# Performance work log

Measured on AMD Instinct MI355X. Metric: run time of the kernel, lower is better.

Reference implementation:

```python
import jax, jax.numpy as jnp
import numpy as np

N = 65536          # nodes
E = 1048576        # edges
IN_C = 128
HID_C = 32
HEADS = 4
OUT_C = 64
NEG_SLOPE = 0.2
EPS = 1e-16


def gat_conv(x, edge_index, W, att_src, att_dst, bias, heads, out_c, concat):
    """PyG-style GATConv. x: [N, F_in]; edge_index: [2, E] (row=src, col=dst).
    W: [F_in, heads*out_c]; att_src/att_dst: [heads, out_c]; bias: [heads*out_c] or [out_c]."""
    src, dst = edge_index[0], edge_index[1]
    n = x.shape[0]
    h = (x @ W).reshape(n, heads, out_c)                      # [N, H, C]
    a_src = jnp.einsum('nhc,hc->nh', h, att_src)              # [N, H]
    a_dst = jnp.einsum('nhc,hc->nh', h, att_dst)              # [N, H]
    alpha = a_src[src] + a_dst[dst]                           # [E, H]
    alpha = jax.nn.leaky_relu(alpha, NEG_SLOPE)
    # segment softmax over incoming edges of each destination node
    amax = jax.ops.segment_max(alpha, dst, num_segments=n)    # [N, H]
    alpha = jnp.exp(alpha - amax[dst])
    denom = jax.ops.segment_sum(alpha, dst, num_segments=n)   # [N, H]
    alpha = alpha / (denom[dst] + EPS)
    # weighted scatter-add aggregation
    msgs = alpha[:, :, None] * h[src]                         # [E, H, C]
    out = jax.ops.segment_sum(msgs, dst, num_segments=n)      # [N, H, C]
    if concat:
        out = out.reshape(n, heads * out_c)
    else:
        out = out.mean(axis=1)
    return out + bias


def setup_inputs() -> dict:
    key = jax.random.key(0)
    ks = jax.random.split(key, 10)
    s_in = 1.0 / np.sqrt(IN_C)
    s_h = 1.0 / np.sqrt(HEADS * HID_C)
    x = jax.random.normal(ks[0], (N, IN_C), dtype=jnp.float32)
    edge_index = jax.random.randint(ks[1], (2, E), 0, N, dtype=jnp.int64)
    W1 = jax.random.normal(ks[2], (IN_C, HEADS * HID_C), dtype=jnp.float32) * s_in
    att_src1 = jax.random.normal(ks[3], (HEADS, HID_C), dtype=jnp.float32) * s_h
    att_dst1 = jax.random.normal(ks[4], (HEADS, HID_C), dtype=jnp.float32) * s_h
    b1 = jnp.zeros((HEADS * HID_C,), dtype=jnp.float32)
    W2 = jax.random.normal(ks[5], (HEADS * HID_C, OUT_C), dtype=jnp.float32) * s_h
    att_src2 = jax.random.normal(ks[6], (1, OUT_C), dtype=jnp.float32) * s_h
    att_dst2 = jax.random.normal(ks[7], (1, OUT_C), dtype=jnp.float32) * s_h
    b2 = jnp.zeros((OUT_C,), dtype=jnp.float32)
    return {"x": x, "edge_index": edge_index, "W1": W1, "att_src1": att_src1,
            "att_dst1": att_dst1, "b1": b1, "W2": W2, "att_src2": att_src2,
            "att_dst2": att_dst2, "b2": b2}


def reference(x, edge_index, W1, att_src1, att_dst1, b1, W2, att_src2, att_dst2, b2):
    # dropout is identity in eval mode
    h = gat_conv(x, edge_index, W1, att_src1, att_dst1, b1, HEADS, HID_C, concat=True)
    h = jax.nn.sigmoid(h)
    h = gat_conv(h, edge_index, W2, att_src2, att_dst2, b2, 1, OUT_C, concat=True)
    return jax.nn.sigmoid(h)
```

## Files before the change

kernel.cpp:

```cpp
#include <hip/hip_runtime.h>
#include <hip/hip_fp16.h>

#define N_NODES 65536
#define N_EDGES 1048576
#define NBUCK 256
#define PBLOCKS 1024
#define EPB (N_EDGES / PBLOCKS)
#define K4CAP 6144
constexpr float NEG = 0.2f;
constexpr float EPS_ = 1e-16f;
constexpr float WSHIFT = 2.7725887f;

typedef __attribute__((ext_vector_type(8))) short bf16x8;
typedef __attribute__((ext_vector_type(4))) float f32x4;

__device__ __forceinline__ unsigned short f2bf(float f) {
    unsigned int u = __float_as_uint(f);
    return (unsigned short)((u + 0x7fffu + ((u >> 16) & 1u)) >> 16);
}
__device__ __forceinline__ unsigned short f2h(float f) {
    __half_raw r = __half_raw(__float2half(f));
    return r.x;
}
__device__ __forceinline__ __half2 u2h2(unsigned int u) {
    union { unsigned int u; __half2 h; } c; c.u = u; return c.h;
}
__device__ __forceinline__ unsigned int h22u(__half2 h) {
    union { unsigned int u; __half2 h; } c; c.h = h; return c.u;
}
__device__ __forceinline__ float lrelu_exp_s(float l) {
    return __expf(fmaxf(l, NEG * l) - WSHIFT);
}


__global__ __launch_bounds__(256) void coarse_hist(const int* __restrict__ ei,
                                                   int* __restrict__ hist_mat) {
    __shared__ int h[NBUCK];
    int t = threadIdx.x;
    h[t] = 0;
    __syncthreads();
    int base = blockIdx.x * EPB;
    #pragma unroll
    for (int i = 0; i < EPB / 256; ++i) {
        int d = ei[N_EDGES + base + i * 256 + t];
        atomicAdd(&h[d >> 8], 1);
    }
    __syncthreads();
    hist_mat[t * PBLOCKS + blockIdx.x] = h[t];
}

__global__ __launch_bounds__(1024) void scan_a(const int* __restrict__ in,
                                               int* __restrict__ out,
                                               int* __restrict__ bsum) {
    __shared__ int sm[1024];
    int t = threadIdx.x, i = blockIdx.x * 1024 + t;
    int v = in[i];
    sm[t] = v;
    __syncthreads();
    for (int off = 1; off < 1024; off <<= 1) {
        int u = (t >= off) ? sm[t - off] : 0;
        __syncthreads();
        sm[t] += u;
        __syncthreads();
    }
    out[i] = sm[t] - v;
    if (t == 1023) bsum[blockIdx.x] = sm[t];
}

__global__ __launch_bounds__(256) void scan_b(int* __restrict__ bsum) {
    __shared__ int sm[256];
    int t = threadIdx.x;
    int v = bsum[t];
    sm[t] = v;
    __syncthreads();
    for (int off = 1; off < 256; off <<= 1) {
        int u = (t >= off) ? sm[t - off] : 0;
        __syncthreads();
        sm[t] += u;
        __syncthreads();
    }
    bsum[t] = sm[t] - v;
}

__global__ __launch_bounds__(1024) void scan_c(int* __restrict__ arr,
                                               const int* __restrict__ bsum) {
    int i = blockIdx.x * 1024 + threadIdx.x;
    arr[i] += bsum[blockIdx.x];
}

__global__ __launch_bounds__(256) void partition_kernel(const int* __restrict__ ei,
                                                        const int* __restrict__ cursor_mat,
                                                        unsigned int* __restrict__ edge_part) {
    __shared__ int h[NBUCK];
    __shared__ int start[NBUCK];
    __shared__ int cur[NBUCK];
    __shared__ int gcur[NBUCK];
    __shared__ unsigned int stage[EPB];
    int t = threadIdx.x;
    h[t] = 0;
    gcur[t] = cursor_mat[t * PBLOCKS + blockIdx.x];
    __syncthreads();
    unsigned int ent[EPB / 256];
    int base = blockIdx.x * EPB;
    #pragma unroll
    for (int i = 0; i < EPB / 256; ++i) {
        int e = base + i * 256 + t;
        int s = ei[e], d = ei[N_EDGES + e];
        ent[i] = ((unsigned int)s << 16) | (unsigned int)d;
        atomicAdd(&h[d >> 8], 1);
    }
    __syncthreads();
    int v = h[t];
    start[t] = v;
    __syncthreads();
    for (int off = 1; off < 256; off <<= 1) {
        int u = (t >= off) ? start[t - off] : 0;
        __syncthreads();
        start[t] += u;
        __syncthreads();
    }
    int excl = start[t] - v;
    start[t] = excl;
    cur[t] = excl;
    __syncthreads();
    #pragma unroll
    for (int i = 0; i < EPB / 256; ++i) {
        int b = (int)((ent[i] & 0xffffu) >> 8);
        int slot = atomicAdd(&cur[b], 1);
        stage[slot] = ent[i];
    }
    __syncthreads();
    int s0 = t * (EPB / 256);
    #pragma unroll
    for (int i = 0; i < EPB / 256; ++i) {
        unsigned int p = stage[s0 + i];
        int b = (int)((p & 0xffffu) >> 8);
        edge_part[gcur[b] + (s0 + i - start[b])] = p;
    }
}

__global__ __launch_bounds__(1024) void finalize_kernel(const unsigned int* __restrict__ edge_part,
                                                        const int* __restrict__ cursor_mat,
                                                        int* __restrict__ row_ptr,
                                                        unsigned short* __restrict__ csr16) {
    __shared__ int h[256];
    __shared__ int sc[256];
    __shared__ int cur[256];
    __shared__ unsigned short stage[K4CAP];
    int t = threadIdx.x;
    int b = blockIdx.x;
    if (b == NBUCK - 1 && t == 0) row_ptr[N_NODES] = N_EDGES;
    int cs = cursor_mat[b * PBLOCKS];
    int ce = (b == NBUCK - 1) ? N_EDGES : cursor_mat[(b + 1) * PBLOCKS];
    int cnt = ce - cs;
    if (t < 256) h[t] = 0;
    __syncthreads();
    for (int i = t; i < cnt; i += 1024)
        atomicAdd(&h[edge_part[cs + i] & 0xffu], 1);
    __syncthreads();
    int v = 0;
    if (t < 256) { v = h[t]; sc[t] = v; }
    __syncthreads();
    for (int off = 1; off < 256; off <<= 1) {
        int u = (t < 256 && t >= off) ? sc[t - off] : 0;
        __syncthreads();
        if (t < 256) sc[t] += u;
        __syncthreads();
    }
    if (t < 256) {
        int excl = sc[t] - v;
        row_ptr[b * 256 + t] = cs + excl;
        cur[t] = excl;
    }
    __syncthreads();
    if (cnt <= K4CAP) {
        for (int i = t; i < cnt; i += 1024) {
            unsigned int p = edge_part[cs + i];
            int slot = atomicAdd(&cur[p & 0xffu], 1);
            stage[slot] = (unsigned short)(p >> 16);
        }
        __syncthreads();
        for (int i = t; i < cnt; i += 1024)
            csr16[cs + i] = stage[i];
    } else {
        for (int i = t; i < cnt; i += 1024) {
            unsigned int p = edge_part[cs + i];
            int slot = atomicAdd(&cur[p & 0xffu], 1);
            csr16[cs + slot] = (unsigned short)(p >> 16);
        }
    }
}


__global__ __launch_bounds__(256) void gemm1_mfma(const float* __restrict__ X,
                                                  const float* __restrict__ W,
                                                  unsigned short* __restrict__ H) {
    constexpr int OUTC = 128;
    constexpr int NT = OUTC / 16;
    extern __shared__ unsigned short Wl[];
    int t = threadIdx.x;
    for (int idx = t; idx < OUTC * 128; idx += 256) {
        int j = idx & 7;
        int ln = (idx >> 3) & 63;
        int fc = idx >> 9;
        int kc = fc & 3, ct = fc >> 2;
        int k = kc * 32 + (ln >> 4) * 8 + j;
        int n = ct * 16 + (ln & 15);
        Wl[idx] = (unsigned short)f2bf(W[k * OUTC + n]);
    }
    __syncthreads();
    int wave = t >> 6, lane = t & 63;
    int m = lane & 15, quad = lane >> 4;
    int node_base = blockIdx.x * 64 + wave * 16;
    const float* xrow = X + (size_t)(node_base + m) * 128 + quad * 8;
    bf16x8 a[4];
    #pragma unroll
    for (int kc = 0; kc < 4; ++kc) {
        float4 u = *(const float4*)(xrow + kc * 32);
        float4 v = *(const float4*)(xrow + kc * 32 + 4);
        bf16x8 af;
        af[0] = (short)f2bf(u.x); af[1] = (short)f2bf(u.y);
        af[2] = (short)f2bf(u.z); af[3] = (short)f2bf(u.w);
        af[4] = (short)f2bf(v.x); af[5] = (short)f2bf(v.y);
        af[6] = (short)f2bf(v.z); af[7] = (short)f2bf(v.w);
        a[kc] = af;
    }
    #pragma unroll
    for (int ct = 0; ct < NT; ++ct) {
        f32x4 acc = {0.f, 0.f, 0.f, 0.f};
        #pragma unroll
        for (int kc = 0; kc < 4; ++kc) {
            bf16x8 bfr = *(const bf16x8*)(Wl + ((ct * 4 + kc) * 64 + lane) * 8);
            acc = __builtin_amdgcn_mfma_f32_16x16x32_bf16(a[kc], bfr, acc, 0, 0, 0);
        }
        #pragma unroll
        for (int r = 0; r < 4; ++r) {
            int row = quad * 4 + r;
            H[(size_t)(node_base + row) * OUTC + ct * 16 + m] = f2h(acc[r]);
        }
    }
}


__global__ __launch_bounds__(256) void gemm2_mfma(const unsigned short* __restrict__ X,
                                                  const float* __restrict__ W,
                                                  unsigned short* __restrict__ H) {
    constexpr int OUTC = 64;
    constexpr int NT = OUTC / 16;
    extern __shared__ unsigned short Wl[];
    int t = threadIdx.x;
    for (int idx = t; idx < OUTC * 128; idx += 256) {
        int j = idx & 7;
        int ln = (idx >> 3) & 63;
        int fc = idx >> 9;
        int kc = fc & 3, ct = fc >> 2;
        int k = kc * 32 + (ln >> 4) * 8 + j;
        int n = ct * 16 + (ln & 15);
        Wl[idx] = (unsigned short)f2bf(W[k * OUTC + n]);
    }
    __syncthreads();
    int wave = t >> 6, lane = t & 63;
    int m = lane & 15, quad = lane >> 4;
    int node_base = blockIdx.x * 64 + wave * 16;
    const unsigned short* xrow = X + (size_t)(node_base + m) * 128 + quad * 8;
    bf16x8 a[4];
    #pragma unroll
    for (int kc = 0; kc < 4; ++kc) a[kc] = *(const bf16x8*)(xrow + kc * 32);
    #pragma unroll
    for (int ct = 0; ct < NT; ++ct) {
        f32x4 acc = {0.f, 0.f, 0.f, 0.f};
        #pragma unroll
        for (int kc = 0; kc < 4; ++kc) {
            bf16x8 bfr = *(const bf16x8*)(Wl + ((ct * 4 + kc) * 64 + lane) * 8);
            acc = __builtin_amdgcn_mfma_f32_16x16x32_bf16(a[kc], bfr, acc, 0, 0, 0);
        }
        #pragma unroll
        for (int r = 0; r < 4; ++r) {
            int row = quad * 4 + r;
            H[(size_t)(node_base + row) * OUTC + ct * 16 + m] = f2h(acc[r]);
        }
    }
}


__global__ __launch_bounds__(256) void att1_kernel(const unsigned int* __restrict__ h1u,
                                                   const float* __restrict__ as_w,
                                                   const float* __restrict__ ad_w,
                                                   float* __restrict__ a_src,
                                                   float* __restrict__ a_dst) {
    int wave = (blockIdx.x * 256 + threadIdx.x) >> 6;
    int lane = threadIdx.x & 63;
    __half2 p = u2h2(h1u[wave * 64 + lane]);
    float h0 = __low2float(p), h1v = __high2float(p);
    float2 sw = *(const float2*)(as_w + lane * 2);
    float2 dw = *(const float2*)(ad_w + lane * 2);
    float ps = h0 * sw.x + h1v * sw.y;
    float pd = h0 * dw.x + h1v * dw.y;
    #pragma unroll
    for (int m = 1; m < 16; m <<= 1) {
        ps += __shfl_xor(ps, m);
        pd += __shfl_xor(pd, m);
    }
    if ((lane & 15) == 0) {
        a_src[wave * 4 + (lane >> 4)] = ps;
        a_dst[wave * 4 + (lane >> 4)] = pd;
    }
}

__global__ __launch_bounds__(256) void att2_kernel(const __half* __restrict__ h2h,
                                                   const float* __restrict__ as_w,
                                                   const float* __restrict__ ad_w,
                                                   float* __restrict__ a_src,
                                                   float* __restrict__ a_dst) {
    int wave = (blockIdx.x * 256 + threadIdx.x) >> 6;
    int lane = threadIdx.x & 63;
    float v = __half2float(h2h[wave * 64 + lane]);
    float ps = v * as_w[lane];
    float pd = v * ad_w[lane];
    #pragma unroll
    for (int m = 1; m < 64; m <<= 1) {
        ps += __shfl_xor(ps, m);
        pd += __shfl_xor(pd, m);
    }
    if (lane == 0) {
        a_src[wave] = ps;
        a_dst[wave] = pd;
    }
}


__global__ __launch_bounds__(256) void agg1_kernel(const int* __restrict__ row_ptr,
                                                   const unsigned short* __restrict__ csr16,
                                                   const unsigned int* __restrict__ h1u,
                                                   const float* __restrict__ a_src,
                                                   const float* __restrict__ a_dst,
                                                   const float* __restrict__ b1,
                                                   unsigned short* __restrict__ x2) {
    int wave = (blockIdx.x * 256 + threadIdx.x) >> 6;
    int lane = threadIdx.x & 63;
    int half = lane >> 5;
    int ln = lane & 31;
    int n = wave * 2 + half;
    int j8 = ln & 7;
    int whead = ln >> 3;
    int sub = ln >> 4;
    int col = ln & 15;
    int hd_c = col >> 2;
    int rbase = half * 32 + hd_c * 8 + sub;
    float adw = a_dst[n * 4 + whead];
    int e = row_ptr[n], end = row_ptr[n + 1];
    __half2 acc0 = u2h2(0u), acc1 = u2h2(0u), acc2 = u2h2(0u), acc3 = u2h2(0u);
    float denom = 0.f;
    while (e < end) {
        int mb = end - e;
        if (mb > 8) mb = 8;
        int s_l = (int)csr16[e + (j8 < mb ? j8 : 0)];
        float l = a_src[s_l * 4 + whead] + adw;
        float wv = (j8 < mb) ? lrelu_exp_s(l) : 0.f;
        denom += wv;
        unsigned int pack = ((unsigned int)f2h(wv) << 16) | (unsigned int)s_l;
        #pragma unroll
        for (int g = 0; g < 4; ++g) {
            unsigned int pk = __shfl(pack, rbase + g * 2);
            unsigned int wu = pk >> 16;
            __half2 w2 = u2h2(wu | (wu << 16));
            unsigned int s = pk & 0xffffu;
            uint4 hv = *(const uint4*)(h1u + s * 64 + col * 4);
            acc0 = __hfma2(w2, u2h2(hv.x), acc0);
            acc1 = __hfma2(w2, u2h2(hv.y), acc1);
            acc2 = __hfma2(w2, u2h2(hv.z), acc2);
            acc3 = __hfma2(w2, u2h2(hv.w), acc3);
        }
        e += 8;
    }
    acc0 = __hadd2(acc0, u2h2(__shfl_xor(h22u(acc0), 16)));
    acc1 = __hadd2(acc1, u2h2(__shfl_xor(h22u(acc1), 16)));
    acc2 = __hadd2(acc2, u2h2(__shfl_xor(h22u(acc2), 16)));
    acc3 = __hadd2(acc3, u2h2(__shfl_xor(h22u(acc3), 16)));
    #pragma unroll
    for (int m = 1; m < 8; m <<= 1) denom += __shfl_xor(denom, m);
    float dfin = __shfl(denom, half * 32 + hd_c * 8);
    if (sub == 0) {
        float inv = 1.f / (dfin + EPS_);
        int c0 = col * 8;
        float v[8];
        v[0] = __low2float(acc0); v[1] = __high2float(acc0);
        v[2] = __low2float(acc1); v[3] = __high2float(acc1);
        v[4] = __low2float(acc2); v[5] = __high2float(acc2);
        v[6] = __low2float(acc3); v[7] = __high2float(acc3);
        unsigned int o[4];
        #pragma unroll
        for (int i = 0; i < 4; ++i) {
            float u0 = v[2 * i] * inv + b1[c0 + 2 * i];
            float u1 = v[2 * i + 1] * inv + b1[c0 + 2 * i + 1];
            u0 = 1.f / (1.f + __expf(-u0));
            u1 = 1.f / (1.f + __expf(-u1));
            o[i] = (unsigned int)f2bf(u0) | ((unsigned int)f2bf(u1) << 16);
        }
        *(uint4*)(x2 + (size_t)n * 128 + c0) = make_uint4(o[0], o[1], o[2], o[3]);
    }
}

__global__ __launch_bounds__(256) void agg2_kernel(const int* __restrict__ row_ptr,
                                                   const unsigned short* __restrict__ csr16,
                                                   const unsigned int* __restrict__ h2u,
                                                   const float* __restrict__ a_src,
                                                   const float* __restrict__ a_dst,
                                                   const float* __restrict__ b2,
                                                   float* __restrict__ out) {
    int wave = (blockIdx.x * 256 + threadIdx.x) >> 6;
    int lane = threadIdx.x & 63;
    int half = lane >> 5;
    int ln = lane & 31;
    int n = wave * 2 + half;
    int j8 = ln & 7;
    int sub = (ln >> 3) & 3;
    int col = ln & 7;
    int rbase = half * 32 + sub;
    float ad = a_dst[n];
    int e = row_ptr[n], end = row_ptr[n + 1];
    __half2 acc0 = u2h2(0u), acc1 = u2h2(0u), acc2 = u2h2(0u), acc3 = u2h2(0u);
    float denom = 0.f;
    while (e < end) {
        int mb = end - e;
        if (mb > 8) mb = 8;
        int s_l = (int)csr16[e + (j8 < mb ? j8 : 0)];
        float l = a_src[s_l] + ad;
        float wv = (j8 < mb) ? lrelu_exp_s(l) : 0.f;
        denom += wv;
        unsigned int pack = ((unsigned int)f2h(wv) << 16) | (unsigned int)s_l;
        #pragma unroll
        for (int g = 0; g < 2; ++g) {
            unsigned int pk = __shfl(pack, rbase + g * 4);
            unsigned int wu = pk >> 16;
            __half2 w2 = u2h2(wu | (wu << 16));
            unsigned int s = pk & 0xffffu;
            uint4 hv = *(const uint4*)(h2u + s * 32 + col * 4);
            acc0 = __hfma2(w2, u2h2(hv.x), acc0);
            acc1 = __hfma2(w2, u2h2(hv.y), acc1);
            acc2 = __hfma2(w2, u2h2(hv.z), acc2);
            acc3 = __hfma2(w2, u2h2(hv.w), acc3);
        }
        e += 8;
    }
    #pragma unroll
    for (int m = 8; m < 32; m <<= 1) {
        acc0 = __hadd2(acc0, u2h2(__shfl_xor(h22u(acc0), m)));
        acc1 = __hadd2(acc1, u2h2(__shfl_xor(h22u(acc1), m)));
        acc2 = __hadd2(acc2, u2h2(__shfl_xor(h22u(acc2), m)));
        acc3 = __hadd2(acc3, u2h2(__shfl_xor(h22u(acc3), m)));
    }
    #pragma unroll
    for (int m = 1; m < 8; m <<= 1) denom += __shfl_xor(denom, m);
    if (sub == 0) {
        float inv = 1.f / (denom + EPS_);
        int c0 = col * 8;
        float v[8];
        v[0] = __low2float(acc0); v[1] = __high2float(acc0);
        v[2] = __low2float(acc1); v[3] = __high2float(acc1);
        v[4] = __low2float(acc2); v[5] = __high2float(acc2);
        v[6] = __low2float(acc3); v[7] = __high2float(acc3);
        float o[8];
        #pragma unroll
        for (int i = 0; i < 8; ++i) {
            float u = v[i] * inv + b2[c0 + i];
            o[i] = 1.f / (1.f + __expf(-u));
        }
        float4* dst = (float4*)(out + (size_t)n * 64 + c0);
        dst[0] = make_float4(o[0], o[1], o[2], o[3]);
        dst[1] = make_float4(o[4], o[5], o[6], o[7]);
    }
}


extern "C" void kernel_launch(void* const* d_in, const int* in_sizes, int n_in,
                              void* d_out, int out_size, void* d_ws, size_t ws_size,
                              hipStream_t stream) {
    (void)in_sizes; (void)n_in; (void)out_size; (void)ws_size;
    const float* x   = (const float*)d_in[0];
    const int*   ei  = (const int*)d_in[1];
    const float* W1  = (const float*)d_in[2];
    const float* as1 = (const float*)d_in[3];
    const float* ad1 = (const float*)d_in[4];
    const float* b1  = (const float*)d_in[5];
    const float* W2  = (const float*)d_in[6];
    const float* as2 = (const float*)d_in[7];
    const float* ad2 = (const float*)d_in[8];
    const float* b2  = (const float*)d_in[9];
    float* out = (float*)d_out;

    char* p = (char*)d_ws;
    auto alloc = [&](size_t bytes) -> void* {
        void* r = (void*)p;
        p += (bytes + 255) & ~(size_t)255;
        return r;
    };
    int* hist_mat   = (int*)alloc((size_t)NBUCK * PBLOCKS * 4);
    int* cursor_mat = (int*)alloc((size_t)NBUCK * PBLOCKS * 4);
    int* bsum       = (int*)alloc(256 * 4);
    unsigned int* edge_part = (unsigned int*)alloc((size_t)N_EDGES * 4);
    int* row_ptr    = (int*)alloc((size_t)(N_NODES + 1) * 4);
    unsigned short* csr16 = (unsigned short*)alloc((size_t)N_EDGES * 2);
    unsigned short* h1 = (unsigned short*)alloc((size_t)N_NODES * 128 * 2);
    float* a_src1   = (float*)alloc((size_t)N_NODES * 4 * 4);
    float* a_dst1   = (float*)alloc((size_t)N_NODES * 4 * 4);
    unsigned short* x2 = (unsigned short*)alloc((size_t)N_NODES * 128 * 2);
    unsigned short* h2 = (unsigned short*)alloc((size_t)N_NODES * 64 * 2);
    float* a_src2   = (float*)alloc((size_t)N_NODES * 4);
    float* a_dst2   = (float*)alloc((size_t)N_NODES * 4);

    coarse_hist<<<PBLOCKS, 256, 0, stream>>>(ei, hist_mat);
    scan_a<<<NBUCK * PBLOCKS / 1024, 1024, 0, stream>>>(hist_mat, cursor_mat, bsum);
    scan_b<<<1, 256, 0, stream>>>(bsum);
    scan_c<<<NBUCK * PBLOCKS / 1024, 1024, 0, stream>>>(cursor_mat, bsum);
    partition_kernel<<<PBLOCKS, 256, 0, stream>>>(ei, cursor_mat, edge_part);
    finalize_kernel<<<NBUCK, 1024, 0, stream>>>(edge_part, cursor_mat, row_ptr, csr16);

    gemm1_mfma<<<N_NODES / 64, 256, 128 * 128 * 2, stream>>>(x, W1, h1);
    att1_kernel<<<N_NODES / 4, 256, 0, stream>>>((const unsigned int*)h1, as1, ad1, a_src1, a_dst1);
    agg1_kernel<<<N_NODES / 8, 256, 0, stream>>>(row_ptr, csr16, (const unsigned int*)h1,
                                                 a_src1, a_dst1, b1, x2);

    gemm2_mfma<<<N_NODES / 64, 256, 128 * 64 * 2, stream>>>(x2, W2, h2);
    att2_kernel<<<N_NODES / 4, 256, 0, stream>>>((const __half*)h2, as2, ad2, a_src2, a_dst2);
    agg2_kernel<<<N_NODES / 8, 256, 0, stream>>>(row_ptr, csr16, (const unsigned int*)h2,
                                                 a_src2, a_dst2, b2, out);
}
```

Before: 244.9 us.

## Fuse attention scores into GEMMs, merge histogram launch, prefetch aggregation loads

Attention logits a_src/a_dst are now computed inside the MFMA GEMM epilogues from fp32 accumulators, which removes the separate att1/att2 kernels that re-read h. The coarse histogram runs as extra blocks in the same launch as gemm1. scan_b is folded into scan_c, where each block sums the preceding block totals itself. The aggregation loops are software-pipelined: gathers are issued before the next chunk's weights are computed, to hide latency. Costs are more registers in the GEMMs and a mixed-role launch whose histogram blocks still request the GEMM's large shared allocation.

```diff
diff --git a/kernel.cpp b/kernel.cpp
--- a/kernel.cpp
+++ b/kernel.cpp
@@ -7,6 +7,7 @@
 #define PBLOCKS 1024
 #define EPB (N_EDGES / PBLOCKS)
 #define K4CAP 6144
+#define GB1 (N_NODES / 64)
 constexpr float NEG = 0.2f;
 constexpr float EPS_ = 1e-16f;
 constexpr float WSHIFT = 2.7725887f;
@@ -32,22 +33,6 @@
     return __expf(fmaxf(l, NEG * l) - WSHIFT);
 }
 
-
-__global__ __launch_bounds__(256) void coarse_hist(const int* __restrict__ ei,
-                                                   int* __restrict__ hist_mat) {
-    __shared__ int h[NBUCK];
-    int t = threadIdx.x;
-    h[t] = 0;
-    __syncthreads();
-    int base = blockIdx.x * EPB;
-    #pragma unroll
-    for (int i = 0; i < EPB / 256; ++i) {
-        int d = ei[N_EDGES + base + i * 256 + t];
-        atomicAdd(&h[d >> 8], 1);
-    }
-    __syncthreads();
-    hist_mat[t * PBLOCKS + blockIdx.x] = h[t];
-}
 
 __global__ __launch_bounds__(1024) void scan_a(const int* __restrict__ in,
                                                int* __restrict__ out,
@@ -67,25 +52,19 @@
     if (t == 1023) bsum[blockIdx.x] = sm[t];
 }
 
-__global__ __launch_bounds__(256) void scan_b(int* __restrict__ bsum) {
-    __shared__ int sm[256];
-    int t = threadIdx.x;
-    int v = bsum[t];
-    sm[t] = v;
-    __syncthreads();
-    for (int off = 1; off < 256; off <<= 1) {
-        int u = (t >= off) ? sm[t - off] : 0;
-        __syncthreads();
-        sm[t] += u;
-        __syncthreads();
-    }
-    bsum[t] = sm[t] - v;
-}
-
 __global__ __launch_bounds__(1024) void scan_c(int* __restrict__ arr,
                                                const int* __restrict__ bsum) {
-    int i = blockIdx.x * 1024 + threadIdx.x;
-    arr[i] += bsum[blockIdx.x];
+    __shared__ int partial[4];
+    int t = threadIdx.x;
+    if (t < 256) {
+        int v = (t < (int)blockIdx.x) ? bsum[t] : 0;
+        #pragma unroll
+        for (int msk = 1; msk < 64; msk <<= 1) v += __shfl_xor(v, msk);
+        if ((t & 63) == 0) partial[t >> 6] = v;
+    }
+    __syncthreads();
+    int pref = partial[0] + partial[1] + partial[2] + partial[3];
+    arr[blockIdx.x * 1024 + t] += pref;
 }
 
 __global__ __launch_bounds__(256) void partition_kernel(const int* __restrict__ ei,
@@ -192,21 +171,42 @@
 }
 
 
-__global__ __launch_bounds__(256) void gemm1_mfma(const float* __restrict__ X,
+__global__ __launch_bounds__(256) void gemm1_hist(const float* __restrict__ X,
                                                   const float* __restrict__ W,
-                                                  unsigned short* __restrict__ H) {
+                                                  const float* __restrict__ as_w,
+                                                  const float* __restrict__ ad_w,
+                                                  const int* __restrict__ ei,
+                                                  unsigned short* __restrict__ H,
+                                                  float* __restrict__ a_src,
+                                                  float* __restrict__ a_dst,
+                                                  int* __restrict__ hist_mat) {
+    extern __shared__ unsigned short Wl[];
+    int t = threadIdx.x;
+    if (blockIdx.x >= GB1) {
+        int* hs = (int*)Wl;
+        int pb = blockIdx.x - GB1;
+        hs[t] = 0;
+        __syncthreads();
+        int base = pb * EPB;
+        #pragma unroll
+        for (int i = 0; i < EPB / 256; ++i) {
+            int d = ei[N_EDGES + base + i * 256 + t];
+            atomicAdd(&hs[d >> 8], 1);
+        }
+        __syncthreads();
+        hist_mat[t * PBLOCKS + pb] = hs[t];
+        return;
+    }
     constexpr int OUTC = 128;
     constexpr int NT = OUTC / 16;
-    extern __shared__ unsigned short Wl[];
-    int t = threadIdx.x;
     for (int idx = t; idx < OUTC * 128; idx += 256) {
         int j = idx & 7;
         int ln = (idx >> 3) & 63;
         int fc = idx >> 9;
         int kc = fc & 3, ct = fc >> 2;
         int k = kc * 32 + (ln >> 4) * 8 + j;
-        int n = ct * 16 + (ln & 15);
-        Wl[idx] = (unsigned short)f2bf(W[k * OUTC + n]);
+        int nn = ct * 16 + (ln & 15);
+        Wl[idx] = (unsigned short)f2bf(W[k * OUTC + nn]);
     }
     __syncthreads();
     int wave = t >> 6, lane = t & 63;
@@ -225,6 +225,14 @@
         af[6] = (short)f2bf(v.z); af[7] = (short)f2bf(v.w);
         a[kc] = af;
     }
+    float asv[NT], adv[NT];
+    #pragma unroll
+    for (int ct = 0; ct < NT; ++ct) {
+        asv[ct] = as_w[ct * 16 + m];
+        adv[ct] = ad_w[ct * 16 + m];
+    }
+    float ps[4][4] = {};
+    float pd[4][4] = {};
     #pragma unroll
     for (int ct = 0; ct < NT; ++ct) {
         f32x4 acc = {0.f, 0.f, 0.f, 0.f};
@@ -233,10 +241,29 @@
             bf16x8 bfr = *(const bf16x8*)(Wl + ((ct * 4 + kc) * 64 + lane) * 8);
             acc = __builtin_amdgcn_mfma_f32_16x16x32_bf16(a[kc], bfr, acc, 0, 0, 0);
         }
+        int hh = ct >> 1;
         #pragma unroll
         for (int r = 0; r < 4; ++r) {
-            int row = quad * 4 + r;
-            H[(size_t)(node_base + row) * OUTC + ct * 16 + m] = f2h(acc[r]);
+            H[(size_t)(node_base + quad * 4 + r) * OUTC + ct * 16 + m] = f2h(acc[r]);
+            ps[r][hh] += acc[r] * asv[ct];
+            pd[r][hh] += acc[r] * adv[ct];
+        }
+    }
+    #pragma unroll
+    for (int r = 0; r < 4; ++r) {
+        #pragma unroll
+        for (int hh = 0; hh < 4; ++hh) {
+            float s = ps[r][hh], d = pd[r][hh];
+            #pragma unroll
+            for (int msk = 1; msk < 16; msk <<= 1) {
+                s += __shfl_xor(s, msk);
+                d += __shfl_xor(d, msk);
+            }
+            if (m == 0) {
+                int node = node_base + quad * 4 + r;
+                a_src[node * 4 + hh] = s;
+                a_dst[node * 4 + hh] = d;
+            }
         }
     }
 }
@@ -244,7 +271,11 @@
 
 __global__ __launch_bounds__(256) void gemm2_mfma(const unsigned short* __restrict__ X,
                                                   const float* __restrict__ W,
-                                                  unsigned short* __restrict__ H) {
+                                                  const float* __restrict__ as_w,
+                                                  const float* __restrict__ ad_w,
+                                                  unsigned short* __restrict__ H,
+                                                  float* __restrict__ a_src,
+                                                  float* __restrict__ a_dst) {
     constexpr int OUTC = 64;
     constexpr int NT = OUTC / 16;
     extern __shared__ unsigned short Wl[];
@@ -255,8 +286,8 @@
         int fc = idx >> 9;
         int kc = fc & 3, ct = fc >> 2;
         int k = kc * 32 + (ln >> 4) * 8 + j;
-        int n = ct * 16 + (ln & 15);
-        Wl[idx] = (unsigned short)f2bf(W[k * OUTC + n]);
+        int nn = ct * 16 + (ln & 15);
+        Wl[idx] = (unsigned short)f2bf(W[k * OUTC + nn]);
     }
     __syncthreads();
     int wave = t >> 6, lane = t & 63;
@@ -266,6 +297,14 @@
     bf16x8 a[4];
     #pragma unroll
     for (int kc = 0; kc < 4; ++kc) a[kc] = *(const bf16x8*)(xrow + kc * 32);
+    float asv[NT], adv[NT];
+    #pragma unroll
+    for (int ct = 0; ct < NT; ++ct) {
+        asv[ct] = as_w[ct * 16 + m];
+        adv[ct] = ad_w[ct * 16 + m];
+    }
+    float ps[4] = {};
+    float pd[4] = {};
     #pragma unroll
     for (int ct = 0; ct < NT; ++ct) {
         f32x4 acc = {0.f, 0.f, 0.f, 0.f};
@@ -276,55 +315,24 @@
         }
         #pragma unroll
         for (int r = 0; r < 4; ++r) {
-            int row = quad * 4 + r;
-            H[(size_t)(node_base + row) * OUTC + ct * 16 + m] = f2h(acc[r]);
-        }
-    }
-}
-
-
-__global__ __launch_bounds__(256) void att1_kernel(const unsigned int* __restrict__ h1u,
-                                                   const float* __restrict__ as_w,
-                                                   const float* __restrict__ ad_w,
-                                                   float* __restrict__ a_src,
-                                                   float* __restrict__ a_dst) {
-    int wave = (blockIdx.x * 256 + threadIdx.x) >> 6;
-    int lane = threadIdx.x & 63;
-    __half2 p = u2h2(h1u[wave * 64 + lane]);
-    float h0 = __low2float(p), h1v = __high2float(p);
-    float2 sw = *(const float2*)(as_w + lane * 2);
-    float2 dw = *(const float2*)(ad_w + lane * 2);
-    float ps = h0 * sw.x + h1v * sw.y;
-    float pd = h0 * dw.x + h1v * dw.y;
-    #pragma unroll
-    for (int m = 1; m < 16; m <<= 1) {
-        ps += __shfl_xor(ps, m);
-        pd += __shfl_xor(pd, m);
-    }
-    if ((lane & 15) == 0) {
-        a_src[wave * 4 + (lane >> 4)] = ps;
-        a_dst[wave * 4 + (lane >> 4)] = pd;
-    }
-}
-
-__global__ __launch_bounds__(256) void att2_kernel(const __half* __restrict__ h2h,
-                                                   const float* __restrict__ as_w,
-                                                   const float* __restrict__ ad_w,
-                                                   float* __restrict__ a_src,
-                                                   float* __restrict__ a_dst) {
-    int wave = (blockIdx.x * 256 + threadIdx.x) >> 6;
-    int lane = threadIdx.x & 63;
-    float v = __half2float(h2h[wave * 64 + lane]);
-    float ps = v * as_w[lane];
-    float pd = v * ad_w[lane];
-    #pragma unroll
-    for (int m = 1; m < 64; m <<= 1) {
-        ps += __shfl_xor(ps, m);
-        pd += __shfl_xor(pd, m);
-    }
-    if (lane == 0) {
-        a_src[wave] = ps;
-        a_dst[wave] = pd;
+            H[(size_t)(node_base + quad * 4 + r) * OUTC + ct * 16 + m] = f2h(acc[r]);
+            ps[r] += acc[r] * asv[ct];
+            pd[r] += acc[r] * adv[ct];
+        }
+    }
+    #pragma unroll
+    for (int r = 0; r < 4; ++r) {
+        float s = ps[r], d = pd[r];
+        #pragma unroll
+        for (int msk = 1; msk < 16; msk <<= 1) {
+            s += __shfl_xor(s, msk);
+            d += __shfl_xor(d, msk);
+        }
+        if (m == 0) {
+            int node = node_base + quad * 4 + r;
+            a_src[node] = s;
+            a_dst[node] = d;
+        }
     }
 }
 
@@ -348,30 +356,62 @@
     int hd_c = col >> 2;
     int rbase = half * 32 + hd_c * 8 + sub;
     float adw = a_dst[n * 4 + whead];
+    const unsigned int* h1c = h1u + col * 4;
+    const float* asw = a_src + whead;
     int e = row_ptr[n], end = row_ptr[n + 1];
     __half2 acc0 = u2h2(0u), acc1 = u2h2(0u), acc2 = u2h2(0u), acc3 = u2h2(0u);
     float denom = 0.f;
-    while (e < end) {
-        int mb = end - e;
-        if (mb > 8) mb = 8;
+    unsigned int cur = 0u;
+    if (e < end) {
+        int mb = end - e; if (mb > 8) mb = 8;
         int s_l = (int)csr16[e + (j8 < mb ? j8 : 0)];
-        float l = a_src[s_l * 4 + whead] + adw;
+        float l = asw[s_l * 4] + adw;
         float wv = (j8 < mb) ? lrelu_exp_s(l) : 0.f;
         denom += wv;
-        unsigned int pack = ((unsigned int)f2h(wv) << 16) | (unsigned int)s_l;
-        #pragma unroll
-        for (int g = 0; g < 4; ++g) {
-            unsigned int pk = __shfl(pack, rbase + g * 2);
-            unsigned int wu = pk >> 16;
-            __half2 w2 = u2h2(wu | (wu << 16));
-            unsigned int s = pk & 0xffffu;
-            uint4 hv = *(const uint4*)(h1u + s * 64 + col * 4);
-            acc0 = __hfma2(w2, u2h2(hv.x), acc0);
-            acc1 = __hfma2(w2, u2h2(hv.y), acc1);
-            acc2 = __hfma2(w2, u2h2(hv.z), acc2);
-            acc3 = __hfma2(w2, u2h2(hv.w), acc3);
-        }
-        e += 8;
+        cur = ((unsigned int)f2h(wv) << 16) | (unsigned int)s_l;
+    }
+    while (e < end) {
+        unsigned int pk0 = __shfl(cur, rbase);
+        unsigned int pk1 = __shfl(cur, rbase + 2);
+        unsigned int pk2 = __shfl(cur, rbase + 4);
+        unsigned int pk3 = __shfl(cur, rbase + 6);
+        uint4 hv0 = *(const uint4*)(h1c + (size_t)(pk0 & 0xffffu) * 64);
+        uint4 hv1 = *(const uint4*)(h1c + (size_t)(pk1 & 0xffffu) * 64);
+        uint4 hv2 = *(const uint4*)(h1c + (size_t)(pk2 & 0xffffu) * 64);
+        uint4 hv3 = *(const uint4*)(h1c + (size_t)(pk3 & 0xffffu) * 64);
+        int en = e + 8;
+        unsigned int nxt = 0u;
+        if (en < end) {
+            int mb = end - en; if (mb > 8) mb = 8;
+            int s_l = (int)csr16[en + (j8 < mb ? j8 : 0)];
+            float l = asw[s_l * 4] + adw;
+            float wv = (j8 < mb) ? lrelu_exp_s(l) : 0.f;
+            denom += wv;
+            nxt = ((unsigned int)f2h(wv) << 16) | (unsigned int)s_l;
+        }
+        unsigned int wu; __half2 w2;
+        wu = pk0 >> 16; w2 = u2h2(wu | (wu << 16));
+        acc0 = __hfma2(w2, u2h2(hv0.x), acc0);
+        acc1 = __hfma2(w2, u2h2(hv0.y), acc1);
+        acc2 = __hfma2(w2, u2h2(hv0.z), acc2);
+        acc3 = __hfma2(w2, u2h2(hv0.w), acc3);
+        wu = pk1 >> 16; w2 = u2h2(wu | (wu << 16));
+        acc0 = __hfma2(w2, u2h2(hv1.x), acc0);
+        acc1 = __hfma2(w2, u2h2(hv1.y), acc1);
+        acc2 = __hfma2(w2, u2h2(hv1.z), acc2);
+        acc3 = __hfma2(w2, u2h2(hv1.w), acc3);
+        wu = pk2 >> 16; w2 = u2h2(wu | (wu << 16));
+        acc0 = __hfma2(w2, u2h2(hv2.x), acc0);
+        acc1 = __hfma2(w2, u2h2(hv2.y), acc1);
+        acc2 = __hfma2(w2, u2h2(hv2.z), acc2);
+        acc3 = __hfma2(w2, u2h2(hv2.w), acc3);
+        wu = pk3 >> 16; w2 = u2h2(wu | (wu << 16));
+        acc0 = __hfma2(w2, u2h2(hv3.x), acc0);
+        acc1 = __hfma2(w2, u2h2(hv3.y), acc1);
+        acc2 = __hfma2(w2, u2h2(hv3.z), acc2);
+        acc3 = __hfma2(w2, u2h2(hv3.w), acc3);
+        cur = nxt;
+        e = en;
     }
     acc0 = __hadd2(acc0, u2h2(__shfl_xor(h22u(acc0), 16)));
     acc1 = __hadd2(acc1, u2h2(__shfl_xor(h22u(acc1), 16)));
@@ -418,30 +458,47 @@
     int col = ln & 7;
     int rbase = half * 32 + sub;
     float ad = a_dst[n];
+    const unsigned int* h2c = h2u + col * 4;
     int e = row_ptr[n], end = row_ptr[n + 1];
     __half2 acc0 = u2h2(0u), acc1 = u2h2(0u), acc2 = u2h2(0u), acc3 = u2h2(0u);
     float denom = 0.f;
-    while (e < end) {
-        int mb = end - e;
-        if (mb > 8) mb = 8;
+    unsigned int cur = 0u;
+    if (e < end) {
+        int mb = end - e; if (mb > 8) mb = 8;
         int s_l = (int)csr16[e + (j8 < mb ? j8 : 0)];
         float l = a_src[s_l] + ad;
         float wv = (j8 < mb) ? lrelu_exp_s(l) : 0.f;
         denom += wv;
-        unsigned int pack = ((unsigned int)f2h(wv) << 16) | (unsigned int)s_l;
-        #pragma unroll
-        for (int g = 0; g < 2; ++g) {
-            unsigned int pk = __shfl(pack, rbase + g * 4);
-            unsigned int wu = pk >> 16;
-            __half2 w2 = u2h2(wu | (wu << 16));
-            unsigned int s = pk & 0xffffu;
-            uint4 hv = *(const uint4*)(h2u + s * 32 + col * 4);
-            acc0 = __hfma2(w2, u2h2(hv.x), acc0);
-            acc1 = __hfma2(w2, u2h2(hv.y), acc1);
-            acc2 = __hfma2(w2, u2h2(hv.z), acc2);
-            acc3 = __hfma2(w2, u2h2(hv.w), acc3);
-        }
-        e += 8;
+        cur = ((unsigned int)f2h(wv) << 16) | (unsigned int)s_l;
+    }
+    while (e < end) {
+        unsigned int pk0 = __shfl(cur, rbase);
+        unsigned int pk1 = __shfl(cur, rbase + 4);
+        uint4 hv0 = *(const uint4*)(h2c + (size_t)(pk0 & 0xffffu) * 32);
+        uint4 hv1 = *(const uint4*)(h2c + (size_t)(pk1 & 0xffffu) * 32);
+        int en = e + 8;
+        unsigned int nxt = 0u;
+        if (en < end) {
+            int mb = end - en; if (mb > 8) mb = 8;
+            int s_l = (int)csr16[en + (j8 < mb ? j8 : 0)];
+            float l = a_src[s_l] + ad;
+            float wv = (j8 < mb) ? lrelu_exp_s(l) : 0.f;
+            denom += wv;
+            nxt = ((unsigned int)f2h(wv) << 16) | (unsigned int)s_l;
+        }
+        unsigned int wu; __half2 w2;
+        wu = pk0 >> 16; w2 = u2h2(wu | (wu << 16));
+        acc0 = __hfma2(w2, u2h2(hv0.x), acc0);
+        acc1 = __hfma2(w2, u2h2(hv0.y), acc1);
+        acc2 = __hfma2(w2, u2h2(hv0.z), acc2);
+        acc3 = __hfma2(w2, u2h2(hv0.w), acc3);
+        wu = pk1 >> 16; w2 = u2h2(wu | (wu << 16));
+        acc0 = __hfma2(w2, u2h2(hv1.x), acc0);
+        acc1 = __hfma2(w2, u2h2(hv1.y), acc1);
+        acc2 = __hfma2(w2, u2h2(hv1.z), acc2);
+        acc3 = __hfma2(w2, u2h2(hv1.w), acc3);
+        cur = nxt;
+        e = en;
     }
     #pragma unroll
     for (int m = 8; m < 32; m <<= 1) {
@@ -509,20 +566,15 @@
     float* a_src2   = (float*)alloc((size_t)N_NODES * 4);
     float* a_dst2   = (float*)alloc((size_t)N_NODES * 4);
 
-    coarse_hist<<<PBLOCKS, 256, 0, stream>>>(ei, hist_mat);
+    gemm1_hist<<<GB1 + PBLOCKS, 256, 128 * 128 * 2, stream>>>(
+        x, W1, as1, ad1, ei, h1, a_src1, a_dst1, hist_mat);
     scan_a<<<NBUCK * PBLOCKS / 1024, 1024, 0, stream>>>(hist_mat, cursor_mat, bsum);
-    scan_b<<<1, 256, 0, stream>>>(bsum);
     scan_c<<<NBUCK * PBLOCKS / 1024, 1024, 0, stream>>>(cursor_mat, bsum);
     partition_kernel<<<PBLOCKS, 256, 0, stream>>>(ei, cursor_mat, edge_part);
     finalize_kernel<<<NBUCK, 1024, 0, stream>>>(edge_part, cursor_mat, row_ptr, csr16);
-
-    gemm1_mfma<<<N_NODES / 64, 256, 128 * 128 * 2, stream>>>(x, W1, h1);
-    att1_kernel<<<N_NODES / 4, 256, 0, stream>>>((const unsigned int*)h1, as1, ad1, a_src1, a_dst1);
     agg1_kernel<<<N_NODES / 8, 256, 0, stream>>>(row_ptr, csr16, (const unsigned int*)h1,
                                                  a_src1, a_dst1, b1, x2);
-
-    gemm2_mfma<<<N_NODES / 64, 256, 128 * 64 * 2, stream>>>(x2, W2, h2);
-    att2_kernel<<<N_NODES / 4, 256, 0, stream>>>((const __half*)h2, as2, ad2, a_src2, a_dst2);
+    gemm2_mfma<<<N_NODES / 64, 256, 128 * 64 * 2, stream>>>(x2, W2, as2, ad2, h2, a_src2, a_dst2);
     agg2_kernel<<<N_NODES / 8, 256, 0, stream>>>(row_ptr, csr16, (const unsigned int*)h2,
                                                  a_src2, a_dst2, b2, out);
 }
```

Result: faster. 221.1 us (-9.7%).
